# Optimization experiments

Hardware: AMD Instinct MI355X
Metric: run time of the kernel (lower is better)

## Reference

```python
import jax, jax.numpy as jnp
import numpy as np

B, T, E, V, A = 8192, 64, 128, 32000, 10


def setup_inputs() -> dict:
    key = jax.random.key(0)
    ks = jax.random.split(key, 8)
    return {
        "utterance": jax.random.randint(ks[0], (B, T), 0, V + 1, dtype=jnp.int64)
            if jax.config.jax_enable_x64 else jax.random.randint(ks[0], (B, T), 0, V + 1).astype(jnp.int32),
        "global_idxes": jnp.arange(B, dtype=jnp.int32),
        "emb_table": jax.random.normal(ks[1], (V + 1, E), jnp.float32) * 0.1,
        "w_ih": jax.random.normal(ks[2], (3 * E, E), jnp.float32) * 0.1,
        "w_hh": jax.random.normal(ks[3], (3 * E, E), jnp.float32) * 0.1,
        "b_ih": jax.random.normal(ks[4], (3 * E,), jnp.float32) * 0.1,
        "b_hh": jax.random.normal(ks[5], (3 * E,), jnp.float32) * 0.1,
        "w_out": jax.random.normal(ks[6], (A, E), jnp.float32) * 0.1,
        "b_out": jax.random.normal(ks[7], (A,), jnp.float32) * 0.1,
    }


def _gru_cell(x, h, w_ih, w_hh, b_ih, b_hh):
    # PyTorch GRUCell math
    gi = x @ w_ih.T + b_ih  # [B, 3E]
    gh = h @ w_hh.T + b_hh  # [B, 3E]
    i_r, i_z, i_n = jnp.split(gi, 3, axis=-1)
    h_r, h_z, h_n = jnp.split(gh, 3, axis=-1)
    r = jax.nn.sigmoid(i_r + h_r)
    z = jax.nn.sigmoid(i_z + h_z)
    n = jnp.tanh(i_n + r * h_n)
    return (1.0 - z) * n + z * h


def reference(utterance, global_idxes, emb_table, w_ih, w_hh, b_ih, b_hh, w_out, b_out):
    bsz = utterance.shape[0]
    h0 = jnp.zeros((bsz, emb_table.shape[1]), emb_table.dtype)
    alive0 = jnp.ones((bsz,), jnp.bool_)

    def step(carry, tok):
        h, out, alive = carry
        emb = emb_table[tok]                      # [B, E] gather
        h = _gru_cell(emb, h, w_ih, w_hh, b_ih, b_hh)
        # output_state only written for rows still alive entering this step
        out = jnp.where(alive[:, None], h, out)
        alive = alive & (tok != 0)                # mark_dead AFTER writing state
        return (h, out, alive), None

    tokens = utterance.T                          # [T, B]
    (_, out_state, _), _ = jax.lax.scan(step, (h0, h0, alive0), tokens)
    logits = out_state @ w_out.T + b_out          # [B, A]
    action_probs = jax.nn.softmax(logits, axis=-1)
    return action_probs
```

## Files before the change

### kernel.cpp

```cpp
#include <hip/hip_runtime.h>
#include <hip/hip_fp16.h>

#define Tt 64
#define Ee 128
#define Aa 10

typedef __attribute__((ext_vector_type(8))) _Float16 half8;
typedef __attribute__((ext_vector_type(4))) float f32x4;

__device__ __forceinline__ float fast_rcp(float x) { return __builtin_amdgcn_rcpf(x); }

__device__ __forceinline__ half8 load_h8(const float* p) {
    f32x4 a = *(const f32x4*)p;
    f32x4 b = *(const f32x4*)(p + 4);
    half8 r;
    r[0] = (_Float16)a[0]; r[1] = (_Float16)a[1]; r[2] = (_Float16)a[2]; r[3] = (_Float16)a[3];
    r[4] = (_Float16)b[0]; r[5] = (_Float16)b[1]; r[6] = (_Float16)b[2]; r[7] = (_Float16)b[3];
    return r;
}

#define MFMA_F16(a, b, c)  __builtin_amdgcn_mfma_f32_16x16x32_f16(a, b, c, 0, 0, 0)

#define SM_BYTES 42624

__global__ __launch_bounds__(512, 2) void gru_fused_kernel(
    const int* __restrict__ utt, const float* __restrict__ emb,
    const float* __restrict__ w_ih, const float* __restrict__ w_hh,
    const float* __restrict__ b_ih, const float* __restrict__ b_hh,
    const float* __restrict__ w_out, const float* __restrict__ b_out,
    float* __restrict__ out) {
    __shared__ __align__(16) char smem[SM_BYTES];
    int* tokb = (int*)smem;
    float* lg = (float*)(smem + 40960);
    int* tstar = (int*)(smem + 42496);
    float* outst = (float*)(smem + 8192);

    const int tid = threadIdx.x;
    const int wv = tid >> 6;
    const int ln = tid & 63;
    const int fn = ln & 15;
    const int kg = ln >> 4;
    const int row0 = blockIdx.x * 32;
    const int gc = wv * 16 + fn;
    const int srow = tid >> 4;
    const int c8 = (tid & 15) << 3;

    if (tid < 32) tstar[tid] = Tt - 1;
    *(f32x4*)(smem + 24576 + tid * 16) = (f32x4){0.f, 0.f, 0.f, 0.f};
    __syncthreads();
    {
        int4 tv = ((const int4*)(utt + (size_t)row0 * Tt))[tid];
        ((int4*)tokb)[tid] = tv;
        int row = tid >> 4;
        int tq = (tid & 15) << 2;
        if (tv.x == 0) atomicMin(&tstar[row], tq);
        if (tv.y == 0) atomicMin(&tstar[row], tq + 1);
        if (tv.z == 0) atomicMin(&tstar[row], tq + 2);
        if (tv.w == 0) atomicMin(&tstar[row], tq + 3);
    }

    half8 wir[4], wiz[4], win[4], whr[4], whz[4], whn[4];
#pragma unroll
    for (int kt = 0; kt < 4; ++kt) {
        int k0 = kt * 32 + kg * 8;
        wir[kt] = load_h8(w_ih + (size_t)gc * Ee + k0);
        wiz[kt] = load_h8(w_ih + (size_t)(128 + gc) * Ee + k0);
        win[kt] = load_h8(w_ih + (size_t)(256 + gc) * Ee + k0);
        whr[kt] = load_h8(w_hh + (size_t)gc * Ee + k0);
        whz[kt] = load_h8(w_hh + (size_t)(128 + gc) * Ee + k0);
        whn[kt] = load_h8(w_hh + (size_t)(256 + gc) * Ee + k0);
    }
    const float bcr = b_ih[gc] + b_hh[gc];
    const float bcz = b_ih[128 + gc] + b_hh[128 + gc];
    const float bin = b_ih[256 + gc];
    const float bhn = b_hh[256 + gc];
    __syncthreads();

    int ts[8];
#pragma unroll
    for (int mt = 0; mt < 2; ++mt)
#pragma unroll
        for (int i = 0; i < 4; ++i) ts[mt * 4 + i] = tstar[mt * 16 + kg * 4 + i];

    {
        int tok = tokb[srow * Tt];
        const float* p = emb + (size_t)tok * Ee + c8;
        f32x4 a = *(const f32x4*)p;
        f32x4 b = *(const f32x4*)(p + 4);
        half8 hx;
#pragma unroll
        for (int j = 0; j < 4; ++j) { hx[j] = (_Float16)a[j]; hx[4 + j] = (_Float16)b[j]; }
        int off = (srow * 256 + c8 * 2) ^ ((srow & 7) << 4);
        *(half8*)(smem + 8192 + off) = hx;
    }
    __syncthreads();

    f32x4 hreg[2], oreg[2];
#pragma unroll
    for (int mt = 0; mt < 2; ++mt) {
        hreg[mt] = (f32x4){0.f, 0.f, 0.f, 0.f};
        oreg[mt] = (f32x4){0.f, 0.f, 0.f, 0.f};
    }

    int cur = 0;
#pragma unroll 1
    for (int t = 0; t < Tt; ++t) {
        f32x4 pa, pb;
        if (t < Tt - 1) {
            int tok = tokb[srow * Tt + t + 1];
            const float* p = emb + (size_t)tok * Ee + c8;
            pa = *(const f32x4*)p;
            pb = *(const f32x4*)(p + 4);
        }

        const char* xb = smem + 8192 + cur * 8192;
        const char* hb = smem + 24576 + cur * 8192;

        f32x4 ar[2], az[2], ain[2], ahn[2];
#pragma unroll
        for (int mt = 0; mt < 2; ++mt) {
            ar[mt] = (f32x4){0.f, 0.f, 0.f, 0.f};
            az[mt] = (f32x4){0.f, 0.f, 0.f, 0.f};
            ain[mt] = (f32x4){0.f, 0.f, 0.f, 0.f};
            ahn[mt] = (f32x4){0.f, 0.f, 0.f, 0.f};
        }
        __builtin_amdgcn_s_setprio(1);
#pragma unroll
        for (int kt = 0; kt < 4; ++kt) {
#pragma unroll
            for (int mt = 0; mt < 2; ++mt) {
                int r = mt * 16 + fn;
                int off = (r * 256 + (kt * 32 + kg * 8) * 2) ^ ((r & 7) << 4);
                half8 xa = *(const half8*)(xb + off);
                half8 ha = *(const half8*)(hb + off);
                ar[mt] = MFMA_F16(xa, wir[kt], ar[mt]);
                ar[mt] = MFMA_F16(ha, whr[kt], ar[mt]);
                az[mt] = MFMA_F16(xa, wiz[kt], az[mt]);
                az[mt] = MFMA_F16(ha, whz[kt], az[mt]);
                ain[mt] = MFMA_F16(xa, win[kt], ain[mt]);
                ahn[mt] = MFMA_F16(ha, whn[kt], ahn[mt]);
            }
        }
        __builtin_amdgcn_s_setprio(0);

        char* hn = smem + 24576 + (cur ^ 1) * 8192;

#pragma unroll
        for (int mt = 0; mt < 2; ++mt) {
#pragma unroll
            for (int i = 0; i < 4; ++i) {
                float pr = ar[mt][i] + bcr;
                float pz = az[mt][i] + bcz;
                float rr = fast_rcp(1.f + __expf(-pr));
                float zz = fast_rcp(1.f + __expf(-pz));
                float pn = ain[mt][i] + bin + rr * (ahn[mt][i] + bhn);
                float e2 = __expf(2.f * pn);
                float nn = 1.f - 2.f * fast_rcp(e2 + 1.f);
                float h = (1.f - zz) * nn + zz * hreg[mt][i];
                hreg[mt][i] = h;
                if (t == ts[mt * 4 + i]) oreg[mt][i] = h;
                if (t < Tt - 1) {
                    int row = mt * 16 + kg * 4 + i;
                    int off = (row * 256 + gc * 2) ^ ((row & 7) << 4);
                    *(_Float16*)(hn + off) = (_Float16)h;
                }
            }
        }
        if (t < Tt - 1) {
            half8 hx;
#pragma unroll
            for (int j = 0; j < 4; ++j) { hx[j] = (_Float16)pa[j]; hx[4 + j] = (_Float16)pb[j]; }
            int off = (srow * 256 + c8 * 2) ^ ((srow & 7) << 4);
            *(half8*)(smem + 8192 + (cur ^ 1) * 8192 + off) = hx;
        }
        __syncthreads();
        cur ^= 1;
    }

#pragma unroll
    for (int mt = 0; mt < 2; ++mt)
#pragma unroll
        for (int i = 0; i < 4; ++i)
            outst[(mt * 16 + kg * 4 + i) * Ee + gc] = oreg[mt][i];
    __syncthreads();

    if (tid < 32 * Aa) {
        int r = tid / Aa, a = tid % Aa;
        const float* wo = w_out + a * Ee;
        const float* os = outst + r * Ee;
        float s = b_out[a];
#pragma unroll
        for (int j = 0; j < Ee; j += 4) {
            f32x4 o = *(const f32x4*)(os + j);
            f32x4 w4 = *(const f32x4*)(wo + j);
            s += o[0] * w4[0] + o[1] * w4[1] + o[2] * w4[2] + o[3] * w4[3];
        }
        lg[r * 12 + a] = s;
    }
    __syncthreads();
    if (tid < 32) {
        float v[Aa];
        float mx = -1e30f;
#pragma unroll
        for (int a = 0; a < Aa; ++a) {
            v[a] = lg[tid * 12 + a];
            mx = fmaxf(mx, v[a]);
        }
        float sum = 0.f;
#pragma unroll
        for (int a = 0; a < Aa; ++a) {
            v[a] = __expf(v[a] - mx);
            sum += v[a];
        }
        float inv = fast_rcp(sum);
#pragma unroll
        for (int a = 0; a < Aa; ++a) out[(size_t)(row0 + tid) * Aa + a] = v[a] * inv;
    }
}

extern "C" void kernel_launch(void* const* d_in, const int* in_sizes, int n_in,
                              void* d_out, int out_size, void* d_ws, size_t ws_size,
                              hipStream_t stream) {
    (void)in_sizes; (void)n_in; (void)d_ws; (void)ws_size; (void)out_size;
    const int* utt = (const int*)d_in[0];
    const float* emb = (const float*)d_in[2];
    const float* wih = (const float*)d_in[3];
    const float* whh = (const float*)d_in[4];
    const float* bih = (const float*)d_in[5];
    const float* bhh = (const float*)d_in[6];
    const float* wout = (const float*)d_in[7];
    const float* bout = (const float*)d_in[8];
    gru_fused_kernel<<<256, 512, 0, stream>>>(utt, emb, wih, whh, bih, bhh, wout, bout,
                                              (float*)d_out);
}
```

Baseline: 138.6 us.

## Halve rows per block to 16 and launch 512 blocks across all CUs

Each block now processes 16 batch rows instead of 32, so the grid doubles from 256 to 512 blocks. With 256 CUs on MI355X the old grid gave one block per CU. The new grid spreads the serial 64-step recurrence across more waves and shrinks LDS and registers per block (launch bounds raised to 4 blocks per CU). The cost is that each block loads and converts the full weight set into registers for only half as many rows, and the MFMA work per wave halves while the per-step barrier and latency chain stay the same.

Result: slower. 313.8 us (+126.5%).

```diff
diff --git a/kernel.cpp b/kernel.cpp
--- a/kernel.cpp
+++ b/kernel.cpp
@@ -6,6 +6,7 @@
 #define Aa 10
 
 typedef __attribute__((ext_vector_type(8))) _Float16 half8;
+typedef __attribute__((ext_vector_type(4))) _Float16 half4;
 typedef __attribute__((ext_vector_type(4))) float f32x4;
 
 __device__ __forceinline__ float fast_rcp(float x) { return __builtin_amdgcn_rcpf(x); }
@@ -21,9 +22,9 @@
 
 #define MFMA_F16(a, b, c)  __builtin_amdgcn_mfma_f32_16x16x32_f16(a, b, c, 0, 0, 0)
 
-#define SM_BYTES 42624
-
-__global__ __launch_bounds__(512, 2) void gru_fused_kernel(
+#define SM_BYTES 21312
+
+__global__ __launch_bounds__(512, 4) void gru_fused_kernel(
     const int* __restrict__ utt, const float* __restrict__ emb,
     const float* __restrict__ w_ih, const float* __restrict__ w_hh,
     const float* __restrict__ b_ih, const float* __restrict__ b_hh,
@@ -31,32 +32,30 @@
     float* __restrict__ out) {
     __shared__ __align__(16) char smem[SM_BYTES];
     int* tokb = (int*)smem;
-    float* lg = (float*)(smem + 40960);
-    int* tstar = (int*)(smem + 42496);
-    float* outst = (float*)(smem + 8192);
+    float* lg = (float*)(smem + 20480);
+    int* tstar = (int*)(smem + 21248);
+    float* outst = (float*)(smem + 4096);
 
     const int tid = threadIdx.x;
     const int wv = tid >> 6;
     const int ln = tid & 63;
     const int fn = ln & 15;
     const int kg = ln >> 4;
-    const int row0 = blockIdx.x * 32;
+    const int row0 = blockIdx.x * 16;
     const int gc = wv * 16 + fn;
-    const int srow = tid >> 4;
-    const int c8 = (tid & 15) << 3;
-
-    if (tid < 32) tstar[tid] = Tt - 1;
-    *(f32x4*)(smem + 24576 + tid * 16) = (f32x4){0.f, 0.f, 0.f, 0.f};
+    const int srow = tid >> 5;
+    const int c4 = (tid & 31) << 2;
+
+    if (tid < 16) tstar[tid] = Tt - 1;
+    *(float2*)(smem + 12288 + tid * 8) = (float2){0.f, 0.f};
     __syncthreads();
     {
-        int4 tv = ((const int4*)(utt + (size_t)row0 * Tt))[tid];
-        ((int4*)tokb)[tid] = tv;
-        int row = tid >> 4;
-        int tq = (tid & 15) << 2;
+        int2 tv = ((const int2*)(utt + (size_t)row0 * Tt))[tid];
+        ((int2*)tokb)[tid] = tv;
+        int row = tid >> 5;
+        int tq = (tid & 31) << 1;
         if (tv.x == 0) atomicMin(&tstar[row], tq);
         if (tv.y == 0) atomicMin(&tstar[row], tq + 1);
-        if (tv.z == 0) atomicMin(&tstar[row], tq + 2);
-        if (tv.w == 0) atomicMin(&tstar[row], tq + 3);
     }
 
     half8 wir[4], wiz[4], win[4], whr[4], whz[4], whn[4];
@@ -76,115 +75,91 @@
     const float bhn = b_hh[256 + gc];
     __syncthreads();
 
-    int ts[8];
-#pragma unroll
-    for (int mt = 0; mt < 2; ++mt)
-#pragma unroll
-        for (int i = 0; i < 4; ++i) ts[mt * 4 + i] = tstar[mt * 16 + kg * 4 + i];
+    int ts[4];
+#pragma unroll
+    for (int i = 0; i < 4; ++i) ts[i] = tstar[kg * 4 + i];
 
     {
         int tok = tokb[srow * Tt];
-        const float* p = emb + (size_t)tok * Ee + c8;
-        f32x4 a = *(const f32x4*)p;
-        f32x4 b = *(const f32x4*)(p + 4);
-        half8 hx;
-#pragma unroll
-        for (int j = 0; j < 4; ++j) { hx[j] = (_Float16)a[j]; hx[4 + j] = (_Float16)b[j]; }
-        int off = (srow * 256 + c8 * 2) ^ ((srow & 7) << 4);
-        *(half8*)(smem + 8192 + off) = hx;
-    }
-    __syncthreads();
-
-    f32x4 hreg[2], oreg[2];
-#pragma unroll
-    for (int mt = 0; mt < 2; ++mt) {
-        hreg[mt] = (f32x4){0.f, 0.f, 0.f, 0.f};
-        oreg[mt] = (f32x4){0.f, 0.f, 0.f, 0.f};
-    }
+        f32x4 a = *(const f32x4*)(emb + (size_t)tok * Ee + c4);
+        half4 hx;
+#pragma unroll
+        for (int j = 0; j < 4; ++j) hx[j] = (_Float16)a[j];
+        int off = (srow * 256 + c4 * 2) ^ ((srow & 7) << 4);
+        *(half4*)(smem + 4096 + off) = hx;
+    }
+    __syncthreads();
+
+    f32x4 hreg = (f32x4){0.f, 0.f, 0.f, 0.f};
+    f32x4 oreg = (f32x4){0.f, 0.f, 0.f, 0.f};
 
     int cur = 0;
 #pragma unroll 1
     for (int t = 0; t < Tt; ++t) {
-        f32x4 pa, pb;
+        f32x4 pa;
         if (t < Tt - 1) {
             int tok = tokb[srow * Tt + t + 1];
-            const float* p = emb + (size_t)tok * Ee + c8;
-            pa = *(const f32x4*)p;
-            pb = *(const f32x4*)(p + 4);
-        }
-
-        const char* xb = smem + 8192 + cur * 8192;
-        const char* hb = smem + 24576 + cur * 8192;
-
-        f32x4 ar[2], az[2], ain[2], ahn[2];
-#pragma unroll
-        for (int mt = 0; mt < 2; ++mt) {
-            ar[mt] = (f32x4){0.f, 0.f, 0.f, 0.f};
-            az[mt] = (f32x4){0.f, 0.f, 0.f, 0.f};
-            ain[mt] = (f32x4){0.f, 0.f, 0.f, 0.f};
-            ahn[mt] = (f32x4){0.f, 0.f, 0.f, 0.f};
-        }
+            pa = *(const f32x4*)(emb + (size_t)tok * Ee + c4);
+        }
+
+        const char* xb = smem + 4096 + cur * 4096;
+        const char* hb = smem + 12288 + cur * 4096;
+
+        f32x4 ar = (f32x4){0.f, 0.f, 0.f, 0.f};
+        f32x4 az = (f32x4){0.f, 0.f, 0.f, 0.f};
+        f32x4 ain = (f32x4){0.f, 0.f, 0.f, 0.f};
+        f32x4 ahn = (f32x4){0.f, 0.f, 0.f, 0.f};
         __builtin_amdgcn_s_setprio(1);
 #pragma unroll
         for (int kt = 0; kt < 4; ++kt) {
-#pragma unroll
-            for (int mt = 0; mt < 2; ++mt) {
-                int r = mt * 16 + fn;
-                int off = (r * 256 + (kt * 32 + kg * 8) * 2) ^ ((r & 7) << 4);
-                half8 xa = *(const half8*)(xb + off);
-                half8 ha = *(const half8*)(hb + off);
-                ar[mt] = MFMA_F16(xa, wir[kt], ar[mt]);
-                ar[mt] = MFMA_F16(ha, whr[kt], ar[mt]);
-                az[mt] = MFMA_F16(xa, wiz[kt], az[mt]);
-                az[mt] = MFMA_F16(ha, whz[kt], az[mt]);
-                ain[mt] = MFMA_F16(xa, win[kt], ain[mt]);
-                ahn[mt] = MFMA_F16(ha, whn[kt], ahn[mt]);
+            int off = (fn * 256 + (kt * 32 + kg * 8) * 2) ^ ((fn & 7) << 4);
+            half8 xa = *(const half8*)(xb + off);
+            half8 ha = *(const half8*)(hb + off);
+            ar = MFMA_F16(xa, wir[kt], ar);
+            ar = MFMA_F16(ha, whr[kt], ar);
+            az = MFMA_F16(xa, wiz[kt], az);
+            az = MFMA_F16(ha, whz[kt], az);
+            ain = MFMA_F16(xa, win[kt], ain);
+            ahn = MFMA_F16(ha, whn[kt], ahn);
+        }
+        __builtin_amdgcn_s_setprio(0);
+
+        char* hn = smem + 12288 + (cur ^ 1) * 4096;
+
+#pragma unroll
+        for (int i = 0; i < 4; ++i) {
+            float pr = ar[i] + bcr;
+            float pz = az[i] + bcz;
+            float rr = fast_rcp(1.f + __expf(-pr));
+            float zz = fast_rcp(1.f + __expf(-pz));
+            float pn = ain[i] + bin + rr * (ahn[i] + bhn);
+            float e2 = __expf(2.f * pn);
+            float nn = 1.f - 2.f * fast_rcp(e2 + 1.f);
+            float h = (1.f - zz) * nn + zz * hreg[i];
+            hreg[i] = h;
+            if (t == ts[i]) oreg[i] = h;
+            if (t < Tt - 1) {
+                int row = kg * 4 + i;
+                int off = (row * 256 + gc * 2) ^ ((row & 7) << 4);
+                *(_Float16*)(hn + off) = (_Float16)h;
             }
         }
-        __builtin_amdgcn_s_setprio(0);
-
-        char* hn = smem + 24576 + (cur ^ 1) * 8192;
-
-#pragma unroll
-        for (int mt = 0; mt < 2; ++mt) {
-#pragma unroll
-            for (int i = 0; i < 4; ++i) {
-                float pr = ar[mt][i] + bcr;
-                float pz = az[mt][i] + bcz;
-                float rr = fast_rcp(1.f + __expf(-pr));
-                float zz = fast_rcp(1.f + __expf(-pz));
-                float pn = ain[mt][i] + bin + rr * (ahn[mt][i] + bhn);
-                float e2 = __expf(2.f * pn);
-                float nn = 1.f - 2.f * fast_rcp(e2 + 1.f);
-                float h = (1.f - zz) * nn + zz * hreg[mt][i];
-                hreg[mt][i] = h;
-                if (t == ts[mt * 4 + i]) oreg[mt][i] = h;
-                if (t < Tt - 1) {
-                    int row = mt * 16 + kg * 4 + i;
-                    int off = (row * 256 + gc * 2) ^ ((row & 7) << 4);
-                    *(_Float16*)(hn + off) = (_Float16)h;
-                }
-            }
-        }
         if (t < Tt - 1) {
-            half8 hx;
-#pragma unroll
-            for (int j = 0; j < 4; ++j) { hx[j] = (_Float16)pa[j]; hx[4 + j] = (_Float16)pb[j]; }
-            int off = (srow * 256 + c8 * 2) ^ ((srow & 7) << 4);
-            *(half8*)(smem + 8192 + (cur ^ 1) * 8192 + off) = hx;
+            half4 hx;
+#pragma unroll
+            for (int j = 0; j < 4; ++j) hx[j] = (_Float16)pa[j];
+            int off = (srow * 256 + c4 * 2) ^ ((srow & 7) << 4);
+            *(half4*)(smem + 4096 + (cur ^ 1) * 4096 + off) = hx;
         }
         __syncthreads();
         cur ^= 1;
     }
 
 #pragma unroll
-    for (int mt = 0; mt < 2; ++mt)
-#pragma unroll
-        for (int i = 0; i < 4; ++i)
-            outst[(mt * 16 + kg * 4 + i) * Ee + gc] = oreg[mt][i];
-    __syncthreads();
-
-    if (tid < 32 * Aa) {
+    for (int i = 0; i < 4; ++i) outst[(kg * 4 + i) * Ee + gc] = oreg[i];
+    __syncthreads();
+
+    if (tid < 16 * Aa) {
         int r = tid / Aa, a = tid % Aa;
         const float* wo = w_out + a * Ee;
         const float* os = outst + r * Ee;
@@ -198,7 +173,7 @@
         lg[r * 12 + a] = s;
     }
     __syncthreads();
-    if (tid < 32) {
+    if (tid < 16) {
         float v[Aa];
         float mx = -1e30f;
 #pragma unroll
@@ -230,6 +205,6 @@
     const float* bhh = (const float*)d_in[6];
     const float* wout = (const float*)d_in[7];
     const float* bout = (const float*)d_in[8];
-    gru_fused_kernel<<<256, 512, 0, stream>>>(utt, emb, wih, whh, bih, bhh, wout, bout,
+    gru_fused_kernel<<<512, 512, 0, stream>>>(utt, emb, wih, whh, bih, bhh, wout, bout,
                                               (float*)d_out);
 }
```
